# Optimization experiments

Measured on AMD Instinct MI355X. Metric: run time of the kernel, lower is better.

The kernel has to match this reference:

```python
import jax, jax.numpy as jnp
import numpy as np

B_SZ, L, H, P, G, N, CS = 2, 2048, 32, 64, 1, 128, 256


def _i8(k, shape):
    return jax.random.randint(k, shape, -127, 128, dtype=jnp.int32).astype(jnp.int8)


def setup_inputs() -> dict:
    key = jax.random.key(0)
    k = jax.random.split(key, 7)
    return {
        "x": _i8(k[0], (B_SZ, L, H, P)),          # quantized int8 activations
        "dt": _i8(k[1], (B_SZ, L, H)),
        "B": _i8(k[2], (B_SZ, L, G, N)),
        "C": _i8(k[3], (B_SZ, L, G, N)),
        "q_A_log": _i8(k[4], (H,)),               # int8 quantized A_log
        "q_D": _i8(k[5], (H,)),                   # int8 quantized D (D_has_hdim=False)
        "dt_bias": jax.random.normal(k[6], (H,), jnp.float32) * 0.1,
        "A_log_scale": jnp.float32(0.02),
        "D_scale": jnp.float32(0.01),
        "dt_scale": jnp.float32(0.03),
        "x_scale": jnp.float32(0.05),
        "B_scale": jnp.float32(0.05),
        "C_scale": jnp.float32(0.05),
    }


def _chunk_scan(x, dt, B, C, q_A_log, q_D, dt_bias,
                A_log_scale, D_scale, dt_scale, x_scale, B_scale, C_scale):
    f32 = jnp.float32
    b, l, h, p = x.shape
    g, n = B.shape[2], B.shape[3]
    cs = CS
    nc = l // cs

    # --- inline dequantization (per-tensor scales, nhead/ndim groups == 0) ---
    xf = x.astype(f32) * x_scale                       # (b, l, h, p)
    dtf = jax.nn.softplus(dt.astype(f32) * dt_scale + dt_bias)   # (b, l, h), dt_limit=(0, inf)
    A = -jnp.exp(q_A_log.astype(f32) * A_log_scale)    # (h,)
    Bf = B.astype(f32) * B_scale                       # (b, l, g, n)
    Cf = C.astype(f32) * C_scale

    # --- chunk the sequence ---
    xc = xf.reshape(b, nc, cs, h, p)
    dtc = dtf.reshape(b, nc, cs, h)
    Bc = Bf.reshape(b, nc, cs, g, n)
    Cc = Cf.reshape(b, nc, cs, g, n)
    rep = h // g
    Bh = jnp.repeat(Bc, rep, axis=3)                   # (b, nc, cs, h, n)
    Ch = jnp.repeat(Cc, rep, axis=3)

    dA = dtc * A                                       # (b, nc, cs, h), <= 0
    cum = jnp.cumsum(dA, axis=2)                       # cumulative log-decay within chunk

    # --- per-chunk states: sum_s exp(cum[-1]-cum[s]) * dt[s] * B[s] (x) x[s] ---
    decay_states = jnp.exp(cum[:, :, -1:, :] - cum)    # (b, nc, cs, h)
    states = jnp.einsum('bzlhn,bzlh,bzlhp->bzhpn', Bh, dtc * decay_states, xc)

    # --- inter-chunk recurrence (sequential scan over chunks) ---
    chunk_decay = jnp.exp(cum[:, :, -1, :])            # (b, nc, h)

    def step(carry, inp):
        s_c, d_c = inp                                 # (b, h, p, n), (b, h)
        new = d_c[:, :, None, None] * carry + s_c
        return new, carry                              # emit state entering this chunk

    states_t = jnp.moveaxis(states, 1, 0)              # (nc, b, h, p, n)
    decay_t = jnp.moveaxis(chunk_decay, 1, 0)          # (nc, b, h)
    final_state, prev_states = jax.lax.scan(
        step, jnp.zeros((b, h, p, n), f32), (states_t, decay_t))
    prev_states = jnp.moveaxis(prev_states, 0, 1)      # (b, nc, h, p, n)

    # --- inter-chunk output: C[l] . state_in * exp(cum[l]) ---
    y_inter = jnp.einsum('bzlhn,bzhpn,bzlh->bzlhp', Ch, prev_states, jnp.exp(cum))

    # --- intra-chunk output: causal (C.B) attention with decay weights ---
    cumT = jnp.moveaxis(cum, 3, 2)                     # (b, nc, h, cs)
    diff = cumT[..., :, None] - cumT[..., None, :]     # (b, nc, h, cs, cs): cum[l]-cum[s]
    mask = jnp.tril(jnp.ones((cs, cs), bool))
    decay_m = jnp.exp(jnp.where(mask, diff, -jnp.inf)) # zero above diagonal, no overflow
    scores = (jnp.einsum('bzlhn,bzshn->bzhls', Ch, Bh)
              * decay_m
              * jnp.moveaxis(dtc, 3, 2)[..., None, :])
    y_intra = jnp.einsum('bzhls,bzshp->bzlhp', scores, xc)

    # --- skip connection D * x (per-head D) ---
    Df = q_D.astype(f32) * D_scale                     # (h,)
    y = (y_intra + y_inter).reshape(b, l, h, p) + xf * Df[None, None, :, None]
    return y


def reference(x, dt, B, C, q_A_log, q_D, dt_bias,
              A_log_scale, D_scale, dt_scale, x_scale, B_scale, C_scale):
    return _chunk_scan(x, dt, B, C, q_A_log, q_D, dt_bias,
                       A_log_scale, D_scale, dt_scale, x_scale, B_scale, C_scale)
```

## Files before the change

kernel.cpp:

```cpp
#include <hip/hip_runtime.h>
#include <math.h>

#define BB 2
#define LSEQ 2048
#define H 32
#define PDIM 64
#define NDIM 128
#define CS 256
#define NC 8

typedef _Float16 half8 __attribute__((ext_vector_type(8)));
typedef _Float16 half4 __attribute__((ext_vector_type(4)));
typedef float floatx4 __attribute__((ext_vector_type(4)));


__device__ __forceinline__ int dot4i8(int a, int b, int c) {
#if __has_builtin(__builtin_amdgcn_sdot4)
    return __builtin_amdgcn_sdot4(a, b, c, false);
#else
    c += ((a << 24) >> 24) * ((b << 24) >> 24);
    c += ((a << 16) >> 24) * ((b << 16) >> 24);
    c += ((a << 8) >> 24) * ((b << 8) >> 24);
    c += (a >> 24) * (b >> 24);
    return c;
#endif
}

__global__ __launch_bounds__(256) void kA1(
    const int* __restrict__ Bm, _Float16* __restrict__ Bt16T)
{
    int t = threadIdx.x;
    int slice = blockIdx.x & 15;
    int zz = blockIdx.x >> 4;
    int z = zz & 7, b = zz >> 3;
    int bz = b * NC + z;
    int nm = t & 15, s8l = t >> 4;
    int n16 = slice & 7, s8 = (slice >> 3) * 16 + s8l;
    const int* bp = Bm + (size_t)(b * LSEQ + z * CS + s8 * 8) * NDIM + n16 * 16 + nm;
    half8 v;
#pragma unroll
    for (int j = 0; j < 8; ++j) v[j] = (_Float16)(float)bp[(size_t)j * NDIM];
    *(half8*)(Bt16T + ((size_t)(bz * 8 + n16) * 32 + s8) * 128 + nm * 8) = v;
}

#define P16_STRIDE 4360
__global__ __launch_bounds__(256, 4) void k013(
    const int* __restrict__ dt, const int* __restrict__ qA, const float* __restrict__ dt_bias,
    const float* __restrict__ A_scale_p, const float* __restrict__ dt_scale_p,
    const int* __restrict__ xq, const float* __restrict__ xs_p, const float* __restrict__ Bs_p,
    const _Float16* __restrict__ Bt16T,
    float* __restrict__ cum, float* __restrict__ cAg, float* __restrict__ cdecay,
    signed char* __restrict__ x8, _Float16* __restrict__ statesF16)
{
    __shared__ float cumS[CS];
    __shared__ float cB[CS];
    __shared__ float wsum[4];
    __shared__ _Float16 xcS[P16_STRIDE + 31 * 136 + 136];
    int t = threadIdx.x;
    int half = blockIdx.x & 1;
    int id = blockIdx.x >> 1;
    int h = id & 31, z = (id >> 5) & 7, b = id >> 8;
    int bz = b * NC + z, bzh = bz * H + h;
    int lane6 = t & 63, w = t >> 6;

    float A = -__expf((float)qA[h] * (*A_scale_p));
    float raw = (float)dt[(size_t)(b * LSEQ + z * CS + t) * H + h];
    float xin = raw * (*dt_scale_p) + dt_bias[h];
    float sp = (xin > 20.f) ? xin : log1pf(__expf(xin));
    float v = sp * A;
#pragma unroll
    for (int off = 1; off < 64; off <<= 1) {
        float u = __shfl_up(v, off, 64);
        if (lane6 >= off) v += u;
    }
    if (lane6 == 63) wsum[w] = v;
    __syncthreads();
    float add = 0.f;
    for (int wv = 0; wv < w; ++wv) add += wsum[wv];
    float cumv = v + add;
    float cl = wsum[0] + wsum[1] + wsum[2] + wsum[3];
    float xs = *xs_p;
    if (half == 0) {
        cum[(size_t)bzh * CS + t] = cumv;
        cAg[(size_t)bzh * CS + t] = sp * xs;
        if (t == 0) cdecay[bzh] = __expf(cl);
    }
    cumS[t] = cumv;
    cB[t] = sp * __expf(cl - cumv) * xs * (*Bs_p);
    __syncthreads();

    int pq = t & 7, srow = t >> 3;
    int p0 = half * 32 + pq * 4;
    const int* xb = xq + ((size_t)(b * LSEQ + z * CS) * H + h) * PDIM + p0;
    signed char* x8b = x8 + ((size_t)(b * LSEQ + z * CS) * H + h) * PDIM + p0;
    int plocal = pq * 4;
    int pbase = (plocal >> 4) * P16_STRIDE + ((plocal & 15) * 8);
    for (int j = 0; j < 8; ++j) {
        int s = j * 32 + srow;
        int4 w4 = *(const int4*)(xb + (size_t)s * (H * PDIM));
        float c = cB[s];
        int sbase = pbase + (s >> 3) * 136 + (s & 7);
        signed char pk[4];
        int xi[4] = {w4.x, w4.y, w4.z, w4.w};
#pragma unroll
        for (int pp = 0; pp < 4; ++pp) {
            xcS[sbase + pp * 8] = (_Float16)((float)xi[pp] * c);
            pk[pp] = (signed char)xi[pp];
        }
        *(int*)(x8b + (size_t)s * (H * PDIM)) = *(int*)pk;
    }
    __syncthreads();

    int m = lane6 & 15, q = lane6 >> 4;
    int p16l = w & 1, ntb = (w >> 1) * 4;
    const _Float16* abase = xcS + p16l * P16_STRIDE + m * 8;
    const _Float16* bbase = Bt16T + (size_t)(bz * 8) * 32 * 128 + m * 8;
    floatx4 acc[4] = {};
    for (int kk = 0; kk < 8; ++kk) {
        if (cl - cumS[kk * 32 + 31] < -30.f) continue;
        int s8k = kk * 4 + q;
        half8 a = *(const half8*)(abase + s8k * 136);
#pragma unroll
        for (int nt = 0; nt < 4; ++nt) {
            half8 bf = *(const half8*)(bbase + ((size_t)(ntb + nt) * 32 + s8k) * 128);
            acc[nt] = __builtin_amdgcn_mfma_f32_16x16x32_f16(a, bf, acc[nt], 0, 0, 0);
        }
    }
    int p16g = half * 2 + p16l;
    _Float16* sb = statesF16 + (size_t)bzh * 8192;
#pragma unroll
    for (int nt = 0; nt < 4; ++nt)
#pragma unroll
        for (int rr = 0; rr < 4; ++rr)
            sb[(size_t)(p16g * 16 + (ntb + nt) * 2 + (m >> 3)) * 128 + (q * 4 + rr) * 8 + (m & 7)] =
                (_Float16)(acc[nt][rr] * 0.0625f);
}

__global__ __launch_bounds__(256) void k4kA2(
    const float* __restrict__ cdecay, const _Float16* __restrict__ statesF16,
    _Float16* __restrict__ statesHT,
    const int* __restrict__ Bm, const int* __restrict__ Cm,
    const float* __restrict__ Bs_p, const float* __restrict__ Cs_p,
    _Float16* __restrict__ CBh, _Float16* __restrict__ C16T)
{
    __shared__ int Bi[64][33];
    __shared__ int Ci[64][33];
    int t = threadIdx.x;
    if (blockIdx.x < 512) {
        int idx = blockIdx.x * 256 + t;
        int off4 = (idx & 2047) * 4;
        int h = (idx >> 11) & 31, b = idx >> 16;
        floatx4 carry = {};
        for (int z = 0; z < NC; ++z) {
            int bzh = (b * NC + z) * H + h;
            half4 v4 = *(const half4*)(statesF16 + (size_t)bzh * 8192 + off4);
            float d = cdecay[bzh];
            half4 o;
#pragma unroll
            for (int i = 0; i < 4; ++i) o[i] = (_Float16)carry[i];
            *(half4*)(statesHT + (size_t)bzh * 8192 + off4) = o;
#pragma unroll
            for (int i = 0; i < 4; ++i) carry[i] = d * carry[i] + (float)v4[i];
        }
        return;
    }
    int bid2 = blockIdx.x - 512;
    int r = bid2 % 26;
    int zz = bid2 / 26;
    int z = zz & 7, b = zz >> 3;
    int bz = b * NC + z;
    if (r < 10) {
        const int LT[10] = {0,1,1,2,2,2,3,3,3,3};
        const int ST[10] = {0,0,1,0,1,2,0,1,2,3};
        int l0 = LT[r] * 64, s0 = ST[r] * 64;
        const int* Bp = Bm + (size_t)(b * LSEQ + z * CS + s0) * NDIM;
        const int* Cp = Cm + (size_t)(b * LSEQ + z * CS + l0) * NDIM;
        for (int i = t; i < 64 * 32; i += 256) {
            int rr = i >> 5, k = i & 31;
            const int* sb = Bp + rr * NDIM + k * 4;
            const int* sc = Cp + rr * NDIM + k * 4;
            Bi[rr][k] = (sb[0] & 255) | ((sb[1] & 255) << 8) | ((sb[2] & 255) << 16) | ((sb[3] & 255) << 24);
            Ci[rr][k] = (sc[0] & 255) | ((sc[1] & 255) << 8) | ((sc[2] & 255) << 16) | ((sc[3] & 255) << 24);
        }
        __syncthreads();
        float cbscale = (*Bs_p) * (*Cs_p);
        int ll = t & 63, lg = t >> 6;
        int acc[16];
#pragma unroll
        for (int i = 0; i < 16; ++i) acc[i] = 0;
        for (int k = 0; k < 32; ++k) {
            int cw = Ci[ll][k];
#pragma unroll
            for (int si = 0; si < 16; ++si)
                acc[si] = dot4i8(cw, Bi[lg * 16 + si][k], acc[si]);
        }
        int l = l0 + ll;
        int l16 = l >> 4, lm = l & 15;
        int sb8 = (s0 + lg * 16) >> 3;
        _Float16* bp = CBh + ((size_t)(bz * 16 + l16) * 32 + sb8) * 128 + lm * 8;
#pragma unroll
        for (int g = 0; g < 2; ++g) {
            half8 v;
#pragma unroll
            for (int i = 0; i < 8; ++i) v[i] = (_Float16)((float)acc[g * 8 + i] * cbscale);
            *(half8*)(bp + g * 128) = v;
        }
    } else {
        int slice = r - 10;
        int lm = t >> 4, n8 = t & 15;
        const int* cp = Cm + (size_t)(b * LSEQ + z * CS + slice * 16 + lm) * NDIM + n8 * 8;
        int4 c0 = *(const int4*)cp;
        int4 c1 = *(const int4*)(cp + 4);
        half8 v;
        v[0] = (_Float16)(float)c0.x; v[1] = (_Float16)(float)c0.y;
        v[2] = (_Float16)(float)c0.z; v[3] = (_Float16)(float)c0.w;
        v[4] = (_Float16)(float)c1.x; v[5] = (_Float16)(float)c1.y;
        v[6] = (_Float16)(float)c1.z; v[7] = (_Float16)(float)c1.w;
        *(half8*)(C16T + ((size_t)(bz * 16 + slice) * 16 + n8) * 128 + lm * 8) = v;
    }
}

#define XT_PITCH 136
__global__ __launch_bounds__(256, 4) void k56(
    const signed char* __restrict__ x8, const int* __restrict__ qD,
    const float* __restrict__ cum, const float* __restrict__ cAg,
    const _Float16* __restrict__ CBh, const _Float16* __restrict__ C16T,
    const _Float16* __restrict__ statesHT,
    const float* __restrict__ Cs_p, const float* __restrict__ xs_p, const float* __restrict__ Ds_p,
    float* __restrict__ out)
{
    __shared__ float cumL[CS];
    __shared__ __align__(16) char smem[4 * 32 * XT_PITCH * 2];
    _Float16* xT = (_Float16*)smem;
    float (*ep)[65] = (float(*)[65])smem;
    int t = threadIdx.x;
    int par = blockIdx.x & 1;
    int id = blockIdx.x >> 1;
    int h = id & 31, z = (id >> 5) & 7, b = id >> 8;
    int bz = b * NC + z, bzh = bz * H + h;
    cumL[t] = cum[(size_t)bzh * CS + t];
    float cav = cAg[(size_t)bzh * CS + t];

    {
        const signed char* xrow = x8 + ((size_t)(b * LSEQ + z * CS + t) * H + h) * PDIM;
        int s8 = t >> 3, sj = t & 7;
        int4 r4 = *(const int4*)xrow;
        int4 r5 = *(const int4*)(xrow + 16);
        int4 r6 = *(const int4*)(xrow + 32);
        int4 r7 = *(const int4*)(xrow + 48);
        int words[16] = {r4.x, r4.y, r4.z, r4.w, r5.x, r5.y, r5.z, r5.w,
                         r6.x, r6.y, r6.z, r6.w, r7.x, r7.y, r7.z, r7.w};
#pragma unroll
        for (int wi = 0; wi < 16; ++wi) {
            int wv = words[wi];
#pragma unroll
            for (int bi = 0; bi < 4; ++bi) {
                int p = wi * 4 + bi;
                int val = (wv << (24 - 8 * bi)) >> 24;
                xT[((p >> 4) * 32 + s8) * XT_PITCH + (p & 15) * 8 + sj] =
                    (_Float16)((float)val * cav);
            }
        }
    }
    __syncthreads();

    int w = t >> 6, lane = t & 63, m = lane & 15, q = lane >> 4;
    floatx4 acc[2][4] = {};

    const _Float16* shb = statesHT + (size_t)bzh * 8192 + m * 8;
    const _Float16* cbase = C16T + (size_t)bz * 16 * 16 * 128 + m * 8;
    bool interact[2];
#pragma unroll
    for (int jl = 0; jl < 2; ++jl) interact[jl] = (cumL[(4 * par + 8 * jl + w) * 16] > -80.f);
    for (int kk = 0; kk < 4; ++kk) {
        int n8 = kk * 4 + q;
        half8 bf[4];
#pragma unroll
        for (int pt = 0; pt < 4; ++pt)
            bf[pt] = *(const half8*)(shb + (pt * 16 + n8) * 128);
#pragma unroll
        for (int jl = 0; jl < 2; ++jl) {
            if (!interact[jl]) continue;
            int l16 = 4 * par + 8 * jl + w;
            half8 ha = *(const half8*)(cbase + ((size_t)l16 * 16 + n8) * 128);
#pragma unroll
            for (int pt = 0; pt < 4; ++pt)
                acc[jl][pt] = __builtin_amdgcn_mfma_f32_16x16x32_f16(ha, bf[pt], acc[jl][pt], 0, 0, 0);
        }
    }
    float Cs16 = (*Cs_p) * 16.0f;
#pragma unroll
    for (int jl = 0; jl < 2; ++jl)
#pragma unroll
        for (int r = 0; r < 4; ++r) {
            float e = __expf(cumL[(4 * par + 8 * jl + w) * 16 + q * 4 + r]) * Cs16;
#pragma unroll
            for (int pt = 0; pt < 4; ++pt) acc[jl][pt][r] *= e;
        }

    const _Float16* cbtb = CBh + (size_t)bz * 16 * 32 * 128 + m * 8;
    int l16max = 4 * par + 8 + w;
    for (int kk = 0; kk < 8; ++kk) {
        if (l16max < 2 * kk) continue;
        int s8 = kk * 4 + q;
        half8 bf[4];
#pragma unroll
        for (int pt = 0; pt < 4; ++pt)
            bf[pt] = *(const half8*)(xT + (size_t)(pt * 32 + s8) * XT_PITCH + m * 8);
        floatx4 c0 = *(const floatx4*)(&cumL[kk * 32 + q * 8]);
        floatx4 c1 = *(const floatx4*)(&cumL[kk * 32 + q * 8 + 4]);
#pragma unroll
        for (int jl = 0; jl < 2; ++jl) {
            int l16 = 4 * par + 8 * jl + w;
            if (l16 < 2 * kk) continue;
            if (cumL[l16 * 16] - cumL[kk * 32 + 31] < -30.f) continue;
            int lA = l16 * 16 + m;
            float cum_l = cumL[lA];
            half8 cb8 = *(const half8*)(cbtb + ((size_t)l16 * 32 + s8) * 128);
            half8 a;
#pragma unroll
            for (int jj = 0; jj < 8; ++jj) {
                int s = kk * 32 + q * 8 + jj;
                float cls = (jj < 4) ? c0[jj] : c1[jj - 4];
                float wv = (float)cb8[jj] * __expf(cum_l - cls);
                a[jj] = (_Float16)((s <= lA) ? wv : 0.f);
            }
#pragma unroll
            for (int pt = 0; pt < 4; ++pt)
                acc[jl][pt] = __builtin_amdgcn_mfma_f32_16x16x32_f16(a, bf[pt], acc[jl][pt], 0, 0, 0);
        }
    }

    float xsDf = (*xs_p) * ((float)qD[h] * (*Ds_p));
    __syncthreads();
#pragma unroll
    for (int jl = 0; jl < 2; ++jl) {
        int lbase = jl * 64 + w * 16 + q * 4;
#pragma unroll
        for (int r = 0; r < 4; ++r)
#pragma unroll
            for (int pt = 0; pt < 4; ++pt)
                ep[lbase + r][pt * 16 + m] = acc[jl][pt][r];
    }
    __syncthreads();
    {
        int lloc = t >> 1;
        int jl = lloc >> 6, wv = (lloc >> 4) & 3, lm = lloc & 15;
        int l = (4 * par + 8 * jl + wv) * 16 + lm;
        size_t go = ((size_t)(b * LSEQ + z * CS + l) * H + h) * PDIM + (t & 1) * 32;
        const float* er = &ep[lloc][(t & 1) * 32];
        const signed char* xp8 = x8 + go;
#pragma unroll
        for (int it = 0; it < 8; ++it) {
            int xw = *(const int*)(xp8 + it * 4);
            floatx4 vv;
            vv[0] = er[it * 4 + 0] + (float)((xw << 24) >> 24) * xsDf;
            vv[1] = er[it * 4 + 1] + (float)((xw << 16) >> 24) * xsDf;
            vv[2] = er[it * 4 + 2] + (float)((xw << 8) >> 24) * xsDf;
            vv[3] = er[it * 4 + 3] + (float)(xw >> 24) * xsDf;
            *(floatx4*)(out + go + it * 4) = vv;
        }
    }
}

extern "C" void kernel_launch(void* const* d_in, const int* in_sizes, int n_in,
                              void* d_out, int out_size, void* d_ws, size_t ws_size,
                              hipStream_t stream)
{
    const int* xq = (const int*)d_in[0];
    const int* dt = (const int*)d_in[1];
    const int* Bm = (const int*)d_in[2];
    const int* Cm = (const int*)d_in[3];
    const int* qA = (const int*)d_in[4];
    const int* qD = (const int*)d_in[5];
    const float* dt_bias = (const float*)d_in[6];
    const float* A_scale = (const float*)d_in[7];
    const float* D_scale = (const float*)d_in[8];
    const float* dt_scale = (const float*)d_in[9];
    const float* x_scale = (const float*)d_in[10];
    const float* B_scale = (const float*)d_in[11];
    const float* C_scale = (const float*)d_in[12];
    float* out = (float*)d_out;

    char* ws = (char*)d_ws;
    float* cum           = (float*)(ws);
    float* cAg           = (float*)(ws + 524288);
    float* cdecay        = (float*)(ws + 1048576);
    _Float16* CBh        = (_Float16*)(ws + 1050624);
    _Float16* statesF16  = (_Float16*)(ws + 3147776);
    _Float16* statesHT   = (_Float16*)(ws + 11536384);
    _Float16* Bt16T      = (_Float16*)(ws + 19924992);
    _Float16* C16T       = (_Float16*)(ws + 20973568);
    signed char* x8      = (signed char*)(ws + 22022144);

    kA1<<<dim3(256), dim3(256), 0, stream>>>(Bm, Bt16T);
    k013<<<dim3(1024), dim3(256), 0, stream>>>(dt, qA, dt_bias, A_scale, dt_scale,
                                               xq, x_scale, B_scale, Bt16T,
                                               cum, cAg, cdecay, x8, statesF16);
    k4kA2<<<dim3(928), dim3(256), 0, stream>>>(cdecay, statesF16, statesHT,
                                               Bm, Cm, B_scale, C_scale, CBh, C16T);
    k56<<<dim3(1024), dim3(256), 0, stream>>>(x8, qD, cum, cAg, CBh, C16T, statesHT,
                                              C_scale, x_scale, D_scale, out);
}
```

Measured before the change: 156.0 us.

## Fold inter-chunk state recurrence into output kernel and merge state/CB kernels

Removes the separate sequential state-passing pass and its statesHT buffer: the output kernel now rebuilds each chunk's incoming state from the per-chunk states of earlier chunks, weighted by cumulative decays in fp16, and stops early once the decay weight is negligible. The CB/C16T preparation blocks move into the chunk-state kernel as extra blocks sharing a union of shared memory. This drops one launch and one global round trip of the states, at the cost of redundant reads and weighting of prior states in every output block. Accumulating in fp16 also adds some precision risk.

```diff
diff --git a/kernel.cpp b/kernel.cpp
--- a/kernel.cpp
+++ b/kernel.cpp
@@ -44,179 +44,159 @@
 }
 
 #define P16_STRIDE 4360
-__global__ __launch_bounds__(256, 4) void k013(
+__global__ __launch_bounds__(256, 4) void k013A2(
     const int* __restrict__ dt, const int* __restrict__ qA, const float* __restrict__ dt_bias,
     const float* __restrict__ A_scale_p, const float* __restrict__ dt_scale_p,
     const int* __restrict__ xq, const float* __restrict__ xs_p, const float* __restrict__ Bs_p,
     const _Float16* __restrict__ Bt16T,
     float* __restrict__ cum, float* __restrict__ cAg, float* __restrict__ cdecay,
-    signed char* __restrict__ x8, _Float16* __restrict__ statesF16)
-{
-    __shared__ float cumS[CS];
-    __shared__ float cB[CS];
-    __shared__ float wsum[4];
-    __shared__ _Float16 xcS[P16_STRIDE + 31 * 136 + 136];
-    int t = threadIdx.x;
-    int half = blockIdx.x & 1;
-    int id = blockIdx.x >> 1;
-    int h = id & 31, z = (id >> 5) & 7, b = id >> 8;
-    int bz = b * NC + z, bzh = bz * H + h;
-    int lane6 = t & 63, w = t >> 6;
-
-    float A = -__expf((float)qA[h] * (*A_scale_p));
-    float raw = (float)dt[(size_t)(b * LSEQ + z * CS + t) * H + h];
-    float xin = raw * (*dt_scale_p) + dt_bias[h];
-    float sp = (xin > 20.f) ? xin : log1pf(__expf(xin));
-    float v = sp * A;
-#pragma unroll
-    for (int off = 1; off < 64; off <<= 1) {
-        float u = __shfl_up(v, off, 64);
-        if (lane6 >= off) v += u;
-    }
-    if (lane6 == 63) wsum[w] = v;
-    __syncthreads();
-    float add = 0.f;
-    for (int wv = 0; wv < w; ++wv) add += wsum[wv];
-    float cumv = v + add;
-    float cl = wsum[0] + wsum[1] + wsum[2] + wsum[3];
-    float xs = *xs_p;
-    if (half == 0) {
-        cum[(size_t)bzh * CS + t] = cumv;
-        cAg[(size_t)bzh * CS + t] = sp * xs;
-        if (t == 0) cdecay[bzh] = __expf(cl);
-    }
-    cumS[t] = cumv;
-    cB[t] = sp * __expf(cl - cumv) * xs * (*Bs_p);
-    __syncthreads();
-
-    int pq = t & 7, srow = t >> 3;
-    int p0 = half * 32 + pq * 4;
-    const int* xb = xq + ((size_t)(b * LSEQ + z * CS) * H + h) * PDIM + p0;
-    signed char* x8b = x8 + ((size_t)(b * LSEQ + z * CS) * H + h) * PDIM + p0;
-    int plocal = pq * 4;
-    int pbase = (plocal >> 4) * P16_STRIDE + ((plocal & 15) * 8);
-    for (int j = 0; j < 8; ++j) {
-        int s = j * 32 + srow;
-        int4 w4 = *(const int4*)(xb + (size_t)s * (H * PDIM));
-        float c = cB[s];
-        int sbase = pbase + (s >> 3) * 136 + (s & 7);
-        signed char pk[4];
-        int xi[4] = {w4.x, w4.y, w4.z, w4.w};
-#pragma unroll
-        for (int pp = 0; pp < 4; ++pp) {
-            xcS[sbase + pp * 8] = (_Float16)((float)xi[pp] * c);
-            pk[pp] = (signed char)xi[pp];
-        }
-        *(int*)(x8b + (size_t)s * (H * PDIM)) = *(int*)pk;
-    }
-    __syncthreads();
-
-    int m = lane6 & 15, q = lane6 >> 4;
-    int p16l = w & 1, ntb = (w >> 1) * 4;
-    const _Float16* abase = xcS + p16l * P16_STRIDE + m * 8;
-    const _Float16* bbase = Bt16T + (size_t)(bz * 8) * 32 * 128 + m * 8;
-    floatx4 acc[4] = {};
-    for (int kk = 0; kk < 8; ++kk) {
-        if (cl - cumS[kk * 32 + 31] < -30.f) continue;
-        int s8k = kk * 4 + q;
-        half8 a = *(const half8*)(abase + s8k * 136);
-#pragma unroll
-        for (int nt = 0; nt < 4; ++nt) {
-            half8 bf = *(const half8*)(bbase + ((size_t)(ntb + nt) * 32 + s8k) * 128);
-            acc[nt] = __builtin_amdgcn_mfma_f32_16x16x32_f16(a, bf, acc[nt], 0, 0, 0);
-        }
-    }
-    int p16g = half * 2 + p16l;
-    _Float16* sb = statesF16 + (size_t)bzh * 8192;
-#pragma unroll
-    for (int nt = 0; nt < 4; ++nt)
-#pragma unroll
-        for (int rr = 0; rr < 4; ++rr)
-            sb[(size_t)(p16g * 16 + (ntb + nt) * 2 + (m >> 3)) * 128 + (q * 4 + rr) * 8 + (m & 7)] =
-                (_Float16)(acc[nt][rr] * 0.0625f);
-}
-
-__global__ __launch_bounds__(256) void k4kA2(
-    const float* __restrict__ cdecay, const _Float16* __restrict__ statesF16,
-    _Float16* __restrict__ statesHT,
-    const int* __restrict__ Bm, const int* __restrict__ Cm,
-    const float* __restrict__ Bs_p, const float* __restrict__ Cs_p,
+    signed char* __restrict__ x8, _Float16* __restrict__ statesF16,
+    const int* __restrict__ Bm, const int* __restrict__ Cm, const float* __restrict__ Cs_p,
     _Float16* __restrict__ CBh, _Float16* __restrict__ C16T)
 {
-    __shared__ int Bi[64][33];
-    __shared__ int Ci[64][33];
+    __shared__ __align__(16) char USH[19488];
     int t = threadIdx.x;
-    if (blockIdx.x < 512) {
-        int idx = blockIdx.x * 256 + t;
-        int off4 = (idx & 2047) * 4;
-        int h = (idx >> 11) & 31, b = idx >> 16;
-        floatx4 carry = {};
-        for (int z = 0; z < NC; ++z) {
-            int bzh = (b * NC + z) * H + h;
-            half4 v4 = *(const half4*)(statesF16 + (size_t)bzh * 8192 + off4);
-            float d = cdecay[bzh];
-            half4 o;
-#pragma unroll
-            for (int i = 0; i < 4; ++i) o[i] = (_Float16)carry[i];
-            *(half4*)(statesHT + (size_t)bzh * 8192 + off4) = o;
-#pragma unroll
-            for (int i = 0; i < 4; ++i) carry[i] = d * carry[i] + (float)v4[i];
-        }
+    if (blockIdx.x < 1024) {
+        float* cumS   = (float*)USH;
+        float* cB     = (float*)(USH + 1024);
+        float* wsum   = (float*)(USH + 2048);
+        _Float16* xcS = (_Float16*)(USH + 2064);
+        int half = blockIdx.x & 1;
+        int id = blockIdx.x >> 1;
+        int h = id & 31, z = (id >> 5) & 7, b = id >> 8;
+        int bz = b * NC + z, bzh = bz * H + h;
+        int lane6 = t & 63, w = t >> 6;
+
+        float A = -__expf((float)qA[h] * (*A_scale_p));
+        float raw = (float)dt[(size_t)(b * LSEQ + z * CS + t) * H + h];
+        float xin = raw * (*dt_scale_p) + dt_bias[h];
+        float sp = (xin > 20.f) ? xin : log1pf(__expf(xin));
+        float v = sp * A;
+#pragma unroll
+        for (int off = 1; off < 64; off <<= 1) {
+            float u = __shfl_up(v, off, 64);
+            if (lane6 >= off) v += u;
+        }
+        if (lane6 == 63) wsum[w] = v;
+        __syncthreads();
+        float add = 0.f;
+        for (int wv = 0; wv < w; ++wv) add += wsum[wv];
+        float cumv = v + add;
+        float cl = wsum[0] + wsum[1] + wsum[2] + wsum[3];
+        float xs = *xs_p;
+        if (half == 0) {
+            cum[(size_t)bzh * CS + t] = cumv;
+            cAg[(size_t)bzh * CS + t] = sp * xs;
+            if (t == 0) cdecay[bzh] = __expf(cl);
+        }
+        cumS[t] = cumv;
+        cB[t] = sp * __expf(cl - cumv) * xs * (*Bs_p);
+        __syncthreads();
+
+        int pq = t & 7, srow = t >> 3;
+        int p0 = half * 32 + pq * 4;
+        const int* xb = xq + ((size_t)(b * LSEQ + z * CS) * H + h) * PDIM + p0;
+        signed char* x8b = x8 + ((size_t)(b * LSEQ + z * CS) * H + h) * PDIM + p0;
+        int plocal = pq * 4;
+        int pbase = (plocal >> 4) * P16_STRIDE + ((plocal & 15) * 8);
+        for (int j = 0; j < 8; ++j) {
+            int s = j * 32 + srow;
+            int4 w4 = *(const int4*)(xb + (size_t)s * (H * PDIM));
+            float c = cB[s];
+            int sbase = pbase + (s >> 3) * 136 + (s & 7);
+            signed char pk[4];
+            int xi[4] = {w4.x, w4.y, w4.z, w4.w};
+#pragma unroll
+            for (int pp = 0; pp < 4; ++pp) {
+                xcS[sbase + pp * 8] = (_Float16)((float)xi[pp] * c);
+                pk[pp] = (signed char)xi[pp];
+            }
+            *(int*)(x8b + (size_t)s * (H * PDIM)) = *(int*)pk;
+        }
+        __syncthreads();
+
+        int m = lane6 & 15, q = lane6 >> 4;
+        int p16l = w & 1, ntb = (w >> 1) * 4;
+        const _Float16* abase = xcS + p16l * P16_STRIDE + m * 8;
+        const _Float16* bbase = Bt16T + (size_t)(bz * 8) * 32 * 128 + m * 8;
+        floatx4 acc[4] = {};
+        for (int kk = 0; kk < 8; ++kk) {
+            if (cl - cumS[kk * 32 + 31] < -30.f) continue;
+            int s8k = kk * 4 + q;
+            half8 a = *(const half8*)(abase + s8k * 136);
+#pragma unroll
+            for (int nt = 0; nt < 4; ++nt) {
+                half8 bf = *(const half8*)(bbase + ((size_t)(ntb + nt) * 32 + s8k) * 128);
+                acc[nt] = __builtin_amdgcn_mfma_f32_16x16x32_f16(a, bf, acc[nt], 0, 0, 0);
+            }
+        }
+        int p16g = half * 2 + p16l;
+        _Float16* sb = statesF16 + (size_t)bzh * 8192;
+#pragma unroll
+        for (int nt = 0; nt < 4; ++nt)
+#pragma unroll
+            for (int rr = 0; rr < 4; ++rr)
+                sb[(size_t)(p16g * 16 + (ntb + nt) * 2 + (m >> 3)) * 128 + (q * 4 + rr) * 8 + (m & 7)] =
+                    (_Float16)(acc[nt][rr] * 0.0625f);
         return;
     }
-    int bid2 = blockIdx.x - 512;
-    int r = bid2 % 26;
-    int zz = bid2 / 26;
-    int z = zz & 7, b = zz >> 3;
-    int bz = b * NC + z;
-    if (r < 10) {
-        const int LT[10] = {0,1,1,2,2,2,3,3,3,3};
-        const int ST[10] = {0,0,1,0,1,2,0,1,2,3};
-        int l0 = LT[r] * 64, s0 = ST[r] * 64;
-        const int* Bp = Bm + (size_t)(b * LSEQ + z * CS + s0) * NDIM;
-        const int* Cp = Cm + (size_t)(b * LSEQ + z * CS + l0) * NDIM;
-        for (int i = t; i < 64 * 32; i += 256) {
-            int rr = i >> 5, k = i & 31;
-            const int* sb = Bp + rr * NDIM + k * 4;
-            const int* sc = Cp + rr * NDIM + k * 4;
-            Bi[rr][k] = (sb[0] & 255) | ((sb[1] & 255) << 8) | ((sb[2] & 255) << 16) | ((sb[3] & 255) << 24);
-            Ci[rr][k] = (sc[0] & 255) | ((sc[1] & 255) << 8) | ((sc[2] & 255) << 16) | ((sc[3] & 255) << 24);
-        }
-        __syncthreads();
-        float cbscale = (*Bs_p) * (*Cs_p);
-        int ll = t & 63, lg = t >> 6;
-        int acc[16];
-#pragma unroll
-        for (int i = 0; i < 16; ++i) acc[i] = 0;
-        for (int k = 0; k < 32; ++k) {
-            int cw = Ci[ll][k];
-#pragma unroll
-            for (int si = 0; si < 16; ++si)
-                acc[si] = dot4i8(cw, Bi[lg * 16 + si][k], acc[si]);
-        }
-        int l = l0 + ll;
-        int l16 = l >> 4, lm = l & 15;
-        int sb8 = (s0 + lg * 16) >> 3;
-        _Float16* bp = CBh + ((size_t)(bz * 16 + l16) * 32 + sb8) * 128 + lm * 8;
-#pragma unroll
-        for (int g = 0; g < 2; ++g) {
+    {
+        int (*Bi)[33] = (int(*)[33])USH;
+        int (*Ci)[33] = (int(*)[33])(USH + 8448);
+        int bid2 = blockIdx.x - 1024;
+        int r = bid2 % 26;
+        int zz = bid2 / 26;
+        int z = zz & 7, b = zz >> 3;
+        int bz = b * NC + z;
+        if (r < 10) {
+            const int LT[10] = {0,1,1,2,2,2,3,3,3,3};
+            const int ST[10] = {0,0,1,0,1,2,0,1,2,3};
+            int l0 = LT[r] * 64, s0 = ST[r] * 64;
+            const int* Bp = Bm + (size_t)(b * LSEQ + z * CS + s0) * NDIM;
+            const int* Cp = Cm + (size_t)(b * LSEQ + z * CS + l0) * NDIM;
+            for (int i = t; i < 64 * 32; i += 256) {
+                int rr = i >> 5, k = i & 31;
+                const int* sb = Bp + rr * NDIM + k * 4;
+                const int* sc = Cp + rr * NDIM + k * 4;
+                Bi[rr][k] = (sb[0] & 255) | ((sb[1] & 255) << 8) | ((sb[2] & 255) << 16) | ((sb[3] & 255) << 24);
+                Ci[rr][k] = (sc[0] & 255) | ((sc[1] & 255) << 8) | ((sc[2] & 255) << 16) | ((sc[3] & 255) << 24);
+            }
+            __syncthreads();
+            float cbscale = (*Bs_p) * (*Cs_p);
+            int ll = t & 63, lg = t >> 6;
+            int acc[16];
+#pragma unroll
+            for (int i = 0; i < 16; ++i) acc[i] = 0;
+            for (int k = 0; k < 32; ++k) {
+                int cw = Ci[ll][k];
+#pragma unroll
+                for (int si = 0; si < 16; ++si)
+                    acc[si] = dot4i8(cw, Bi[lg * 16 + si][k], acc[si]);
+            }
+            int l = l0 + ll;
+            int l16 = l >> 4, lm = l & 15;
+            int sb8 = (s0 + lg * 16) >> 3;
+            _Float16* bp = CBh + ((size_t)(bz * 16 + l16) * 32 + sb8) * 128 + lm * 8;
+#pragma unroll
+            for (int g = 0; g < 2; ++g) {
+                half8 v;
+#pragma unroll
+                for (int i = 0; i < 8; ++i) v[i] = (_Float16)((float)acc[g * 8 + i] * cbscale);
+                *(half8*)(bp + g * 128) = v;
+            }
+        } else {
+            int slice = r - 10;
+            int lm = t >> 4, n8 = t & 15;
+            const int* cp = Cm + (size_t)(b * LSEQ + z * CS + slice * 16 + lm) * NDIM + n8 * 8;
+            int4 c0 = *(const int4*)cp;
+            int4 c1 = *(const int4*)(cp + 4);
             half8 v;
-#pragma unroll
-            for (int i = 0; i < 8; ++i) v[i] = (_Float16)((float)acc[g * 8 + i] * cbscale);
-            *(half8*)(bp + g * 128) = v;
-        }
-    } else {
-        int slice = r - 10;
-        int lm = t >> 4, n8 = t & 15;
-        const int* cp = Cm + (size_t)(b * LSEQ + z * CS + slice * 16 + lm) * NDIM + n8 * 8;
-        int4 c0 = *(const int4*)cp;
-        int4 c1 = *(const int4*)(cp + 4);
-        half8 v;
-        v[0] = (_Float16)(float)c0.x; v[1] = (_Float16)(float)c0.y;
-        v[2] = (_Float16)(float)c0.z; v[3] = (_Float16)(float)c0.w;
-        v[4] = (_Float16)(float)c1.x; v[5] = (_Float16)(float)c1.y;
-        v[6] = (_Float16)(float)c1.z; v[7] = (_Float16)(float)c1.w;
-        *(half8*)(C16T + ((size_t)(bz * 16 + slice) * 16 + n8) * 128 + lm * 8) = v;
+            v[0] = (_Float16)(float)c0.x; v[1] = (_Float16)(float)c0.y;
+            v[2] = (_Float16)(float)c0.z; v[3] = (_Float16)(float)c0.w;
+            v[4] = (_Float16)(float)c1.x; v[5] = (_Float16)(float)c1.y;
+            v[6] = (_Float16)(float)c1.z; v[7] = (_Float16)(float)c1.w;
+            *(half8*)(C16T + ((size_t)(bz * 16 + slice) * 16 + n8) * 128 + lm * 8) = v;
+        }
     }
 }
 
@@ -224,8 +204,9 @@
 __global__ __launch_bounds__(256, 4) void k56(
     const signed char* __restrict__ x8, const int* __restrict__ qD,
     const float* __restrict__ cum, const float* __restrict__ cAg,
+    const float* __restrict__ cdecay,
     const _Float16* __restrict__ CBh, const _Float16* __restrict__ C16T,
-    const _Float16* __restrict__ statesHT,
+    const _Float16* __restrict__ statesF16,
     const float* __restrict__ Cs_p, const float* __restrict__ xs_p, const float* __restrict__ Ds_p,
     float* __restrict__ out)
 {
@@ -267,25 +248,36 @@
     int w = t >> 6, lane = t & 63, m = lane & 15, q = lane >> 4;
     floatx4 acc[2][4] = {};
 
-    const _Float16* shb = statesHT + (size_t)bzh * 8192 + m * 8;
+    bool interact[2];
+#pragma unroll
+    for (int jl = 0; jl < 2; ++jl) interact[jl] = (cumL[(4 * par + 8 * jl + w) * 16] > -80.f);
     const _Float16* cbase = C16T + (size_t)bz * 16 * 16 * 128 + m * 8;
-    bool interact[2];
-#pragma unroll
-    for (int jl = 0; jl < 2; ++jl) interact[jl] = (cumL[(4 * par + 8 * jl + w) * 16] > -80.f);
-    for (int kk = 0; kk < 4; ++kk) {
-        int n8 = kk * 4 + q;
-        half8 bf[4];
-#pragma unroll
-        for (int pt = 0; pt < 4; ++pt)
-            bf[pt] = *(const half8*)(shb + (pt * 16 + n8) * 128);
-#pragma unroll
-        for (int jl = 0; jl < 2; ++jl) {
-            if (!interact[jl]) continue;
-            int l16 = 4 * par + 8 * jl + w;
-            half8 ha = *(const half8*)(cbase + ((size_t)l16 * 16 + n8) * 128);
-#pragma unroll
-            for (int pt = 0; pt < 4; ++pt)
-                acc[jl][pt] = __builtin_amdgcn_mfma_f32_16x16x32_f16(ha, bf[pt], acc[jl][pt], 0, 0, 0);
+    if (z > 0 && (interact[0] || interact[1])) {
+        const float* cdb = cdecay + (size_t)b * NC * H + h;
+        for (int kk = 0; kk < 4; ++kk) {
+            int n8 = kk * 4 + q;
+            half8 bf[4] = {};
+            float wsc = 1.f;
+            for (int u = z - 1; u >= 0; --u) {
+                if (wsc < 1e-8f) break;
+                _Float16 wh = (_Float16)wsc;
+                const _Float16* sfb = statesF16 + ((size_t)((b * NC + u) * H) + h) * 8192 + m * 8;
+#pragma unroll
+                for (int pt = 0; pt < 4; ++pt) {
+                    half8 fr = *(const half8*)(sfb + (pt * 16 + n8) * 128);
+                    bf[pt] += fr * wh;
+                }
+                wsc *= cdb[(size_t)u * H];
+            }
+#pragma unroll
+            for (int jl = 0; jl < 2; ++jl) {
+                if (!interact[jl]) continue;
+                int l16 = 4 * par + 8 * jl + w;
+                half8 ha = *(const half8*)(cbase + ((size_t)l16 * 16 + n8) * 128);
+#pragma unroll
+                for (int pt = 0; pt < 4; ++pt)
+                    acc[jl][pt] = __builtin_amdgcn_mfma_f32_16x16x32_f16(ha, bf[pt], acc[jl][pt], 0, 0, 0);
+            }
         }
     }
     float Cs16 = (*Cs_p) * 16.0f;
@@ -388,17 +380,15 @@
     float* cdecay        = (float*)(ws + 1048576);
     _Float16* CBh        = (_Float16*)(ws + 1050624);
     _Float16* statesF16  = (_Float16*)(ws + 3147776);
-    _Float16* statesHT   = (_Float16*)(ws + 11536384);
     _Float16* Bt16T      = (_Float16*)(ws + 19924992);
     _Float16* C16T       = (_Float16*)(ws + 20973568);
     signed char* x8      = (signed char*)(ws + 22022144);
 
     kA1<<<dim3(256), dim3(256), 0, stream>>>(Bm, Bt16T);
-    k013<<<dim3(1024), dim3(256), 0, stream>>>(dt, qA, dt_bias, A_scale, dt_scale,
-                                               xq, x_scale, B_scale, Bt16T,
-                                               cum, cAg, cdecay, x8, statesF16);
-    k4kA2<<<dim3(928), dim3(256), 0, stream>>>(cdecay, statesF16, statesHT,
-                                               Bm, Cm, B_scale, C_scale, CBh, C16T);
-    k56<<<dim3(1024), dim3(256), 0, stream>>>(x8, qD, cum, cAg, CBh, C16T, statesHT,
-                                              C_scale, x_scale, D_scale, out);
-}
+    k013A2<<<dim3(1440), dim3(256), 0, stream>>>(dt, qA, dt_bias, A_scale, dt_scale,
+                                                 xq, x_scale, B_scale, Bt16T,
+                                                 cum, cAg, cdecay, x8, statesF16,
+                                                 Bm, Cm, C_scale, CBh, C16T);
+    k56<<<dim3(1024), dim3(256), 0, stream>>>(x8, qD, cum, cAg, cdecay, CBh, C16T,
+                                              statesF16, C_scale, x_scale, D_scale, out);
+}
```

New measurement: 148.6 us, median of 2. -4.8%, faster.
